# Optimization experiments

Measured on AMD Instinct MI355X. Metric: run time of the kernel, lower is better.

Reference implementation:

```python
import jax, jax.numpy as jnp
import numpy as np

N_NODES = 100000   # nodes per node type
N_EDGES = 800000   # edges per edge type
F_IN = 128         # lazy (-1,-1) input feature dim, chosen == hidden
HID = 128          # hidden_channels
OUT = 1            # out_channels
N_LAYERS = 2
B = 256            # batch_size (num graphs)
NEG_SLOPE = 0.2    # GATConv default leaky_relu slope


def setup_inputs() -> dict:
    key = jax.random.key(0)
    ks = jax.random.split(key, 16)
    x_i = jax.random.normal(ks[0], (N_NODES, F_IN), jnp.float32)
    x_j = jax.random.normal(ks[1], (N_NODES, F_IN), jnp.float32)
    ei_ii = jax.random.randint(ks[2], (2, N_EDGES), 0, N_NODES, jnp.int32)
    ei_jj = jax.random.randint(ks[3], (2, N_EDGES), 0, N_NODES, jnp.int32)
    ei_ij = jax.random.randint(ks[4], (2, N_EDGES), 0, N_NODES, jnp.int32)
    ei_ji = jax.random.randint(ks[5], (2, N_EDGES), 0, N_NODES, jnp.int32)
    batch_i = jnp.sort(jax.random.randint(ks[6], (N_NODES,), 0, B, jnp.int32))
    batch_j = jnp.sort(jax.random.randint(ks[7], (N_NODES,), 0, B, jnp.int32))
    s = 1.0 / np.sqrt(HID)
    Ws = jax.random.normal(ks[8], (N_LAYERS, 4, F_IN, HID), jnp.float32) * s
    Wd = jax.random.normal(ks[9], (N_LAYERS, 4, F_IN, HID), jnp.float32) * s
    att_s = jax.random.normal(ks[10], (N_LAYERS, 4, HID), jnp.float32) * s
    att_d = jax.random.normal(ks[11], (N_LAYERS, 4, HID), jnp.float32) * s
    bias = jnp.zeros((N_LAYERS, 4, HID), jnp.float32)
    lin_w = jax.random.normal(ks[12], (HID, OUT), jnp.float32) * s
    lin_b = jnp.zeros((OUT,), jnp.float32)
    return dict(x_i=x_i, x_j=x_j, ei_ii=ei_ii, ei_jj=ei_jj, ei_ij=ei_ij,
                ei_ji=ei_ji, batch_i=batch_i, batch_j=batch_j, Ws=Ws, Wd=Wd,
                att_s=att_s, att_d=att_d, bias=bias, lin_w=lin_w, lin_b=lin_b)


def gat_conv(x_src, x_dst, edge, W_s, W_d, a_s, a_d, b):
    """Single-head GATConv: gather -> edge attention -> segment softmax -> scatter."""
    src, dst = edge[0], edge[1]
    n_dst = x_dst.shape[0]
    hs = x_src @ W_s                      # [Ns, C]
    hd = x_dst @ W_d                      # [Nd, C]
    e = jax.nn.leaky_relu((hs * a_s).sum(-1)[src] + (hd * a_d).sum(-1)[dst],
                          NEG_SLOPE)      # [E]
    m = jax.ops.segment_max(e, dst, num_segments=n_dst)
    m = jnp.where(jnp.isfinite(m), m, 0.0)  # empty segments -> 0
    p = jnp.exp(e - m[dst])
    denom = jax.ops.segment_sum(p, dst, num_segments=n_dst)
    alpha = p / jnp.maximum(denom[dst], 1e-16)
    out = jax.ops.segment_sum(alpha[:, None] * hs[src], dst, num_segments=n_dst)
    return out + b


def mean_pool(x, batch, size):
    s = jax.ops.segment_sum(x, batch, num_segments=size)
    cnt = jax.ops.segment_sum(jnp.ones((x.shape[0],), x.dtype), batch,
                              num_segments=size)
    return s / jnp.maximum(cnt, 1.0)[:, None]


def reference(x_i, x_j, ei_ii, ei_jj, ei_ij, ei_ji, batch_i, batch_j,
              Ws, Wd, att_s, att_d, bias, lin_w, lin_b):
    xi, xj = x_i, x_j
    for l in range(N_LAYERS):
        # edge-type order: 0=inner_i, 1=inner_j, 2=outer_ij, 3=outer_ji
        out_i = (gat_conv(xi, xi, ei_ii, Ws[l, 0], Wd[l, 0], att_s[l, 0], att_d[l, 0], bias[l, 0])
                 + gat_conv(xj, xi, ei_ji, Ws[l, 3], Wd[l, 3], att_s[l, 3], att_d[l, 3], bias[l, 3]))
        out_j = (gat_conv(xj, xj, ei_jj, Ws[l, 1], Wd[l, 1], att_s[l, 1], att_d[l, 1], bias[l, 1])
                 + gat_conv(xi, xj, ei_ij, Ws[l, 2], Wd[l, 2], att_s[l, 2], att_d[l, 2], bias[l, 2]))
        xi, xj = jnp.tanh(out_i), jnp.tanh(out_j)
    p_i = mean_pool(xi, batch_i, B)       # [B, HID]
    p_j = mean_pool(xj, batch_j, B)       # [B, HID]
    x = 0.5 * (p_i + p_j)                 # mean over the stacked pair
    return jax.nn.sigmoid(x @ lin_w + lin_b)
```

## Files before the change

### kernel.cpp

```cpp
#include <hip/hip_runtime.h>


#define NEG_SLOPE 0.2f

typedef __attribute__((ext_vector_type(8))) short short8v;
typedef __attribute__((ext_vector_type(4))) float float4v;
typedef __attribute__((ext_vector_type(2))) float float2v;

__device__ __forceinline__ unsigned short f2bf(float f) {
  unsigned u = __float_as_uint(f);
  unsigned r = (u + 0x7FFFu + ((u >> 16) & 1u)) >> 16;
  return (unsigned short)r;
}
__device__ __forceinline__ unsigned pack2(float a, float b) {
  return (unsigned)f2bf(a) | ((unsigned)f2bf(b) << 16);
}
__device__ __forceinline__ float bflo(unsigned u) {
  return __uint_as_float(u << 16);
}
__device__ __forceinline__ float bfhi(unsigned u) {
  return __uint_as_float(u & 0xFFFF0000u);
}
__device__ __forceinline__ float rl_f(float x, int lane) {
  return __int_as_float(__builtin_amdgcn_readlane(__float_as_int(x), lane));
}
__device__ __forceinline__ int rl_i(int x, int lane) {
  return __builtin_amdgcn_readlane(x, lane);
}

__global__ __launch_bounds__(256) void w_to_bf16t(const float* __restrict__ W,
                                                  unsigned short* __restrict__ Wt) {
  __shared__ float buf[64][129];
  int b = blockIdx.x, t = threadIdx.x;
  const float* w = W + (size_t)b * 16384;
  unsigned short* o = Wt + (size_t)b * 16384;
  for (int h = 0; h < 2; ++h) {
    for (int i = 0; i < 32; ++i) {
      int idx = i * 256 + t;
      buf[idx >> 7][idx & 127] = w[(size_t)(h * 64 + (idx >> 7)) * 128 + (idx & 127)];
    }
    __syncthreads();
    for (int i = 0; i < 32; ++i) {
      int idx = i * 256 + t;
      o[(size_t)(idx >> 6) * 128 + h * 64 + (idx & 63)] = f2bf(buf[idx & 63][idx >> 6]);
    }
    __syncthreads();
  }
}

__global__ void precompute_wa(const float* __restrict__ W,
                              const float* __restrict__ att,
                              float* __restrict__ out) {
  int idx = blockIdx.x;
  int f = threadIdx.x;
  const float* w = W + (size_t)idx * 128 * 128 + (size_t)f * 128;
  const float* a = att + idx * 128;
  float s = 0.f;
  #pragma unroll 8
  for (int h = 0; h < 128; ++h) s += w[h] * a[h];
  out[idx * 128 + f] = s;
}

struct GemmArgs {
  const unsigned short* Wt1; const float* att1;
  unsigned char* Hb1; float* as1;
  const unsigned short* Wt2; const float* att2;
  unsigned char* Hb2; float* as2;
  const float* vdA; const float* vdB;
  float* adA; float* adB;
};

template <int XBF16>
__global__ __launch_bounds__(256) void gemm_dual2(
    const void* __restrict__ X0, const void* __restrict__ X1,
    GemmArgs Ga, GemmArgs Gb, int M) {
  __shared__ unsigned short Xt[64][136];
  __shared__ unsigned short Wt[128][136];
  const int t = threadIdx.x;
  const int row0 = blockIdx.x * 64;
  const void* Xv = blockIdx.y ? X1 : X0;
  const GemmArgs& G = blockIdx.y ? Gb : Ga;

  {
    int r = t >> 2;
    int cq = (t & 3) * 32;
    int gr = row0 + r;
    if (gr >= M) gr = M - 1;
    if (XBF16) {
      const unsigned short* Xb = (const unsigned short*)Xv;
      const uint4* src = (const uint4*)(Xb + (size_t)gr * 128 + cq);
      #pragma unroll
      for (int i = 0; i < 4; ++i) *(uint4*)&Xt[r][cq + i * 8] = src[i];
    } else {
      const float* Xf = (const float*)Xv;
      const float4* src = (const float4*)(Xf + (size_t)gr * 128 + cq);
      #pragma unroll
      for (int i = 0; i < 8; ++i) {
        float4 v = src[i];
        uint2 u;
        u.x = pack2(v.x, v.y);
        u.y = pack2(v.z, v.w);
        *(uint2*)&Xt[r][cq + i * 4] = u;
      }
    }
  }
  {
    int n = t >> 1;
    int kh = (t & 1) * 64;
    const uint4* src = (const uint4*)(G.Wt1 + (size_t)n * 128 + kh);
    #pragma unroll
    for (int i = 0; i < 8; ++i) *(uint4*)&Wt[n][kh + i * 8] = src[i];
  }
  __syncthreads();

  if (t < 128) {
    int r = t & 63;
    const float* vd = (t < 64) ? G.vdA : G.vdB;
    float* adout = (t < 64) ? G.adA : G.adB;
    float sum = 0.f;
    #pragma unroll 4
    for (int k8 = 0; k8 < 16; ++k8) {
      uint4 u = *(const uint4*)&Xt[r][k8 * 8];
      const float* v = vd + k8 * 8;
      sum = fmaf(bflo(u.x), v[0], sum);
      sum = fmaf(bfhi(u.x), v[1], sum);
      sum = fmaf(bflo(u.y), v[2], sum);
      sum = fmaf(bfhi(u.y), v[3], sum);
      sum = fmaf(bflo(u.z), v[4], sum);
      sum = fmaf(bfhi(u.z), v[5], sum);
      sum = fmaf(bflo(u.w), v[6], sum);
      sum = fmaf(bfhi(u.w), v[7], sum);
    }
    int gr = row0 + r;
    if (gr < M) adout[gr] = sum;
  }

  const int lane = t & 63;
  const int wv = t >> 6;
  const int m = lane & 15;
  const int g = lane >> 4;
  const int ws = wv * 16;

  for (int ww = 0; ww < 2; ++ww) {
    if (ww == 1) {
      __syncthreads();
      int n = t >> 1;
      int kh = (t & 1) * 64;
      const uint4* src = (const uint4*)(G.Wt2 + (size_t)n * 128 + kh);
      #pragma unroll
      for (int i = 0; i < 8; ++i) *(uint4*)&Wt[n][kh + i * 8] = src[i];
      __syncthreads();
    }
    const float* att = ww ? G.att2 : G.att1;
    unsigned char* Hb = ww ? G.Hb2 : G.Hb1;
    float* as_ = ww ? G.as2 : G.as1;

    float4v acc[8];
    float4v z = {0.f, 0.f, 0.f, 0.f};
    #pragma unroll
    for (int nt = 0; nt < 8; ++nt) acc[nt] = z;

    #pragma unroll
    for (int ks = 0; ks < 4; ++ks) {
      short8v a = *(const short8v*)&Xt[ws + m][ks * 32 + g * 8];
      #pragma unroll
      for (int nt = 0; nt < 8; ++nt) {
        short8v b = *(const short8v*)&Wt[nt * 16 + m][ks * 32 + g * 8];
        acc[nt] = __builtin_amdgcn_mfma_f32_16x16x32_bf16(a, b, acc[nt], 0, 0, 0);
      }
    }

    {
      float attv[8];
      #pragma unroll
      for (int nt = 0; nt < 8; ++nt) attv[nt] = att[nt * 16 + m];
      #pragma unroll
      for (int r = 0; r < 4; ++r) {
        float s = 0.f;
        #pragma unroll
        for (int nt = 0; nt < 8; ++nt) s = fmaf(acc[nt][r], attv[nt], s);
        #pragma unroll
        for (int off = 1; off < 16; off <<= 1) s += __shfl_xor(s, off);
        if (m == 0) {
          int grow = row0 + ws + g * 4 + r;
          if (grow < M) as_[grow] = s;
        }
      }
    }

    #pragma unroll
    for (int nt = 0; nt < 8; ++nt) {
      #pragma unroll
      for (int r = 0; r < 4; ++r) {
        float v = acc[nt][r];
        float vn = __shfl_xor(v, 1);
        if ((m & 1) == 0) {
          int grow = row0 + ws + g * 4 + r;
          if (grow < M) {
            int pk = __builtin_amdgcn_cvt_pk_fp8_f32(v, vn, 0, false);
            *(unsigned short*)(Hb + (size_t)grow * 128 + nt * 16 + m) =
                (unsigned short)(pk & 0xFFFF);
          }
        }
      }
    }
  }
}

__global__ void hist4(const int* __restrict__ e0, const int* __restrict__ e1,
                      const int* __restrict__ e2, const int* __restrict__ e3,
                      int E, int* __restrict__ deg, int N) {
  int t = blockIdx.y;
  const int* ei = (t == 0) ? e0 : (t == 1) ? e1 : (t == 2) ? e2 : e3;
  int stride = gridDim.x * 256;
  for (int i = blockIdx.x * 256 + threadIdx.x; i < E; i += stride)
    atomicAdd(&deg[t * N + ei[E + i]], 1);
}

__global__ __launch_bounds__(1024) void scan4(const int* __restrict__ deg,
                                              int* __restrict__ rowptr, int N) {
  __shared__ int sums[1024];
  int t = threadIdx.x;
  int ty = blockIdx.x;
  const int* d = deg + (size_t)ty * N;
  int* rp = rowptr + (size_t)ty * (N + 1);
  int chunk = (N + 1023) / 1024;
  int lo = t * chunk;
  int hi = lo + chunk; if (hi > N) hi = N; if (lo > N) lo = N;
  int s = 0;
  for (int i = lo; i < hi; ++i) s += d[i];
  sums[t] = s;
  __syncthreads();
  for (int off = 1; off < 1024; off <<= 1) {
    int add = (t >= off) ? sums[t - off] : 0;
    __syncthreads();
    sums[t] += add;
    __syncthreads();
  }
  int run = (t == 0) ? 0 : sums[t - 1];
  for (int i = lo; i < hi; ++i) {
    rp[i] = run;
    run += d[i];
  }
  if (t == 1023) rp[N] = sums[1023];
}

__global__ void fill4(const int* __restrict__ e0, const int* __restrict__ e1,
                      const int* __restrict__ e2, const int* __restrict__ e3,
                      int E, const int* __restrict__ rowptr,
                      int* __restrict__ fill, int* __restrict__ csrc, int N) {
  int t = blockIdx.y;
  const int* ei = (t == 0) ? e0 : (t == 1) ? e1 : (t == 2) ? e2 : e3;
  int stride = gridDim.x * 256;
  for (int i = blockIdx.x * 256 + threadIdx.x; i < E; i += stride) {
    int d = ei[E + i];
    int s = ei[i];
    int pos = rowptr[(size_t)t * (N + 1) + d] + atomicAdd(&fill[t * N + d], 1);
    csrc[(size_t)t * E + pos] = s;
  }
}

struct PairArgs {
  const int* rA; const int* sA; const unsigned char* hA;
  const float* asA; const float* adA;
  const int* rB; const int* sB; const unsigned char* hB;
  const float* asB; const float* adB;
  const float* biasA; const float* biasB;
};

#define GATH(P_h, idx, dst) {                                           \
  unsigned short uu = *(const unsigned short*)((P_h) + (size_t)(idx) * 128 + lane * 2); \
  dst = __builtin_amdgcn_cvt_pk_f32_fp8((int)uu, false); }

__device__ __forceinline__ void agg_pair(const PairArgs& P, int n, int lane,
                                         float2& outA, float2& outB) {
  int begA = P.rA[n], endA = P.rA[n + 1];
  int begB = P.rB[n], endB = P.rB[n + 1];
  float adA = P.adA[n], adB = P.adB[n];
  float lsA = 0.f, lsB = 0.f;
  float2 aA = make_float2(0.f, 0.f), aB = make_float2(0.f, 0.f);
  int cA = begA, cB = begB;
  while (cA < endA || cB < endB) {
    int kA = cA + lane, kB = cB + lane;
    bool vA = kA < endA;
    bool vB = kB < endB;
    int sA = vA ? P.sA[kA] : 0;
    int sB = vB ? P.sB[kB] : 0;
    float eA = vA ? (P.asA[sA] + adA) : 0.f;
    float eB = vB ? (P.asB[sB] + adB) : 0.f;
    eA = eA > 0.f ? eA : NEG_SLOPE * eA;
    eB = eB > 0.f ? eB : NEG_SLOPE * eB;
    float pA = vA ? __expf(eA) : 0.f;
    float pB = vB ? __expf(eB) : 0.f;
    int cntA = endA - cA; cntA = cntA < 0 ? 0 : (cntA > 64 ? 64 : cntA);
    int cntB = endB - cB; cntB = cntB < 0 ? 0 : (cntB > 64 ? 64 : cntB);
    int cnt = cntA > cntB ? cntA : cntB;
    for (int base = 0; base < cnt; base += 8) {
      float qa0 = rl_f(pA, base + 0), qa1 = rl_f(pA, base + 1);
      float qa2 = rl_f(pA, base + 2), qa3 = rl_f(pA, base + 3);
      float qa4 = rl_f(pA, base + 4), qa5 = rl_f(pA, base + 5);
      float qa6 = rl_f(pA, base + 6), qa7 = rl_f(pA, base + 7);
      float qb0 = rl_f(pB, base + 0), qb1 = rl_f(pB, base + 1);
      float qb2 = rl_f(pB, base + 2), qb3 = rl_f(pB, base + 3);
      float qb4 = rl_f(pB, base + 4), qb5 = rl_f(pB, base + 5);
      float qb6 = rl_f(pB, base + 6), qb7 = rl_f(pB, base + 7);
      int ta0 = rl_i(sA, base + 0), ta1 = rl_i(sA, base + 1);
      int ta2 = rl_i(sA, base + 2), ta3 = rl_i(sA, base + 3);
      int ta4 = rl_i(sA, base + 4), ta5 = rl_i(sA, base + 5);
      int ta6 = rl_i(sA, base + 6), ta7 = rl_i(sA, base + 7);
      int tb0 = rl_i(sB, base + 0), tb1 = rl_i(sB, base + 1);
      int tb2 = rl_i(sB, base + 2), tb3 = rl_i(sB, base + 3);
      int tb4 = rl_i(sB, base + 4), tb5 = rl_i(sB, base + 5);
      int tb6 = rl_i(sB, base + 6), tb7 = rl_i(sB, base + 7);
      float2v ha0, ha1, ha2, ha3, ha4, ha5, ha6, ha7;
      float2v hb0, hb1, hb2, hb3, hb4, hb5, hb6, hb7;
      GATH(P.hA, ta0, ha0) GATH(P.hA, ta1, ha1)
      GATH(P.hA, ta2, ha2) GATH(P.hA, ta3, ha3)
      GATH(P.hA, ta4, ha4) GATH(P.hA, ta5, ha5)
      GATH(P.hA, ta6, ha6) GATH(P.hA, ta7, ha7)
      GATH(P.hB, tb0, hb0) GATH(P.hB, tb1, hb1)
      GATH(P.hB, tb2, hb2) GATH(P.hB, tb3, hb3)
      GATH(P.hB, tb4, hb4) GATH(P.hB, tb5, hb5)
      GATH(P.hB, tb6, hb6) GATH(P.hB, tb7, hb7)
      lsA += ((qa0 + qa1) + (qa2 + qa3)) + ((qa4 + qa5) + (qa6 + qa7));
      lsB += ((qb0 + qb1) + (qb2 + qb3)) + ((qb4 + qb5) + (qb6 + qb7));
      aA.x = fmaf(qa0, ha0[0], aA.x); aA.y = fmaf(qa0, ha0[1], aA.y);
      aA.x = fmaf(qa1, ha1[0], aA.x); aA.y = fmaf(qa1, ha1[1], aA.y);
      aA.x = fmaf(qa2, ha2[0], aA.x); aA.y = fmaf(qa2, ha2[1], aA.y);
      aA.x = fmaf(qa3, ha3[0], aA.x); aA.y = fmaf(qa3, ha3[1], aA.y);
      aA.x = fmaf(qa4, ha4[0], aA.x); aA.y = fmaf(qa4, ha4[1], aA.y);
      aA.x = fmaf(qa5, ha5[0], aA.x); aA.y = fmaf(qa5, ha5[1], aA.y);
      aA.x = fmaf(qa6, ha6[0], aA.x); aA.y = fmaf(qa6, ha6[1], aA.y);
      aA.x = fmaf(qa7, ha7[0], aA.x); aA.y = fmaf(qa7, ha7[1], aA.y);
      aB.x = fmaf(qb0, hb0[0], aB.x); aB.y = fmaf(qb0, hb0[1], aB.y);
      aB.x = fmaf(qb1, hb1[0], aB.x); aB.y = fmaf(qb1, hb1[1], aB.y);
      aB.x = fmaf(qb2, hb2[0], aB.x); aB.y = fmaf(qb2, hb2[1], aB.y);
      aB.x = fmaf(qb3, hb3[0], aB.x); aB.y = fmaf(qb3, hb3[1], aB.y);
      aB.x = fmaf(qb4, hb4[0], aB.x); aB.y = fmaf(qb4, hb4[1], aB.y);
      aB.x = fmaf(qb5, hb5[0], aB.x); aB.y = fmaf(qb5, hb5[1], aB.y);
      aB.x = fmaf(qb6, hb6[0], aB.x); aB.y = fmaf(qb6, hb6[1], aB.y);
      aB.x = fmaf(qb7, hb7[0], aB.x); aB.y = fmaf(qb7, hb7[1], aB.y);
    }
    cA += 64;
    cB += 64;
  }
  float invA = 1.f / fmaxf(lsA, 1e-16f);
  float invB = 1.f / fmaxf(lsB, 1e-16f);
  outA = make_float2(aA.x * invA, aA.y * invA);
  outB = make_float2(aB.x * invB, aB.y * invB);
}

__global__ __launch_bounds__(256) void agg_store2(
    PairArgs P0, unsigned short* __restrict__ out0,
    PairArgs P1, unsigned short* __restrict__ out1, int N) {
  int wave = (blockIdx.x * 256 + threadIdx.x) >> 6;
  int lane = threadIdx.x & 63;
  if (wave >= N) return;
  const PairArgs& P = blockIdx.y ? P1 : P0;
  unsigned short* out = blockIdx.y ? out1 : out0;
  float2 a, b;
  agg_pair(P, wave, lane, a, b);
  float2 b1 = *(const float2*)(P.biasA + lane * 2);
  float2 b2 = *(const float2*)(P.biasB + lane * 2);
  float vx = tanhf(a.x + b.x + b1.x + b2.x);
  float vy = tanhf(a.y + b.y + b1.y + b2.y);
  *(unsigned*)(out + (size_t)wave * 128 + lane * 2) = pack2(vx, vy);
}

__global__ __launch_bounds__(256) void agg_pool2(
    PairArgs P0, const int* __restrict__ batch0, float* __restrict__ pool0,
    PairArgs P1, const int* __restrict__ batch1, float* __restrict__ pool1,
    int N) {
  int wave = (blockIdx.x * 256 + threadIdx.x) >> 6;
  int lane = threadIdx.x & 63;
  if (wave >= N) return;
  const PairArgs& P = blockIdx.y ? P1 : P0;
  const int* batch = blockIdx.y ? batch1 : batch0;
  float* pool = blockIdx.y ? pool1 : pool0;
  float2 a, b;
  agg_pair(P, wave, lane, a, b);
  float2 b1 = *(const float2*)(P.biasA + lane * 2);
  float2 b2 = *(const float2*)(P.biasB + lane * 2);
  float vx = tanhf(a.x + b.x + b1.x + b2.x);
  float vy = tanhf(a.y + b.y + b1.y + b2.y);
  int bb = batch[wave];
  float* p = pool + (size_t)bb * 128 + lane * 2;
  unsafeAtomicAdd(p, vx);
  unsafeAtomicAdd(p + 1, vy);
}

__device__ __forceinline__ int lower_bound_i(const int* __restrict__ a, int n,
                                             int v) {
  int lo = 0, hi = n;
  while (lo < hi) {
    int mid = (lo + hi) >> 1;
    if (a[mid] < v) lo = mid + 1; else hi = mid;
  }
  return lo;
}

__global__ void final_k(const float* __restrict__ pool_i,
                        const int* __restrict__ batch_i,
                        const float* __restrict__ pool_j,
                        const int* __restrict__ batch_j, int N,
                        const float* __restrict__ lin_w,
                        const float* __restrict__ lin_b,
                        float* __restrict__ out) {
  int b = threadIdx.x;
  float ci = (float)(lower_bound_i(batch_i, N, b + 1) -
                     lower_bound_i(batch_i, N, b));
  float cj = (float)(lower_bound_i(batch_j, N, b + 1) -
                     lower_bound_i(batch_j, N, b));
  ci = fmaxf(ci, 1.f);
  cj = fmaxf(cj, 1.f);
  float acc = 0.f;
  #pragma unroll 4
  for (int f = 0; f < 128; ++f) {
    float x = 0.5f * (pool_i[(size_t)b * 128 + f] / ci +
                      pool_j[(size_t)b * 128 + f] / cj);
    acc += x * lin_w[f];
  }
  acc += lin_b[0];
  out[b] = 1.f / (1.f + __expf(-acc));
}

extern "C" void kernel_launch(void* const* d_in, const int* in_sizes, int n_in,
                              void* d_out, int out_size, void* d_ws,
                              size_t ws_size, hipStream_t stream) {
  const float* x_i = (const float*)d_in[0];
  const float* x_j = (const float*)d_in[1];
  const int* ei_arr[4] = {(const int*)d_in[2], (const int*)d_in[3],
                          (const int*)d_in[4], (const int*)d_in[5]};
  const int* batch_i = (const int*)d_in[6];
  const int* batch_j = (const int*)d_in[7];
  const float* Ws = (const float*)d_in[8];
  const float* Wd = (const float*)d_in[9];
  const float* att_s = (const float*)d_in[10];
  const float* att_d = (const float*)d_in[11];
  const float* bias = (const float*)d_in[12];
  const float* lin_w = (const float*)d_in[13];
  const float* lin_b = (const float*)d_in[14];
  float* out = (float*)d_out;

  const int N = in_sizes[0] / 128;
  const int E = in_sizes[2] / 2;
  const size_t NF = (size_t)N * 128;

  char* w = (char*)d_ws;
  auto alloc = [&](size_t bytes) {
    char* p = w;
    w += (bytes + 255) & ~(size_t)255;
    return p;
  };
  unsigned short* bufA_i = (unsigned short*)alloc(NF * 2);
  unsigned short* bufA_j = (unsigned short*)alloc(NF * 2);
  unsigned char* hsb[4];
  for (int c = 0; c < 4; ++c) hsb[c] = (unsigned char*)alloc(NF);
  int* csrc = (int*)alloc((size_t)4 * E * 4);
  int* rowptr = (int*)alloc((size_t)4 * (N + 1) * 4);
  int* deg = (int*)alloc((size_t)4 * N * 4);
  int* fillc = (int*)alloc((size_t)4 * N * 4);
  float* asb[4];
  for (int c = 0; c < 4; ++c) asb[c] = (float*)alloc((size_t)N * 4);
  float* adb[4];
  for (int c = 0; c < 4; ++c) adb[c] = (float*)alloc((size_t)N * 4);
  float* wdad = (float*)alloc(8 * 128 * 4);
  unsigned short* Wst = (unsigned short*)alloc(8 * 16384 * 2);
  float* pool = (float*)alloc(2 * 256 * 128 * 4);
  float* pool_i = pool;
  float* pool_j = pool + 256 * 128;

  w_to_bf16t<<<8, 256, 0, stream>>>(Ws, Wst);
  precompute_wa<<<8, 128, 0, stream>>>(Wd, att_d, wdad);

  hipMemsetAsync(deg, 0, (size_t)4 * N * 4, stream);
  hipMemsetAsync(fillc, 0, (size_t)4 * N * 4, stream);
  dim3 egrid(512, 4);
  hist4<<<egrid, 256, 0, stream>>>(ei_arr[0], ei_arr[1], ei_arr[2], ei_arr[3],
                                   E, deg, N);
  scan4<<<4, 1024, 0, stream>>>(deg, rowptr, N);
  fill4<<<egrid, 256, 0, stream>>>(ei_arr[0], ei_arr[1], ei_arr[2], ei_arr[3],
                                   E, rowptr, fillc, csrc, N);

  hipMemsetAsync(pool, 0, 2 * 256 * 128 * 4, stream);

  const int gemm_blocks = (N + 63) / 64;
  const int nodew_blocks = (N + 3) / 4;

  for (int l = 0; l < 2; ++l) {
    const void* cur_i = (l == 0) ? (const void*)x_i : (const void*)bufA_i;
    const void* cur_j = (l == 0) ? (const void*)x_j : (const void*)bufA_j;
    const size_t L = (size_t)l * 4;

    GemmArgs Ga = {Wst + (L + 0) * 16384, att_s + (L + 0) * 128, hsb[0], asb[0],
                   Wst + (L + 2) * 16384, att_s + (L + 2) * 128, hsb[2], asb[2],
                   wdad + (L + 0) * 128, wdad + (L + 3) * 128, adb[0], adb[3]};
    GemmArgs Gb = {Wst + (L + 1) * 16384, att_s + (L + 1) * 128, hsb[1], asb[1],
                   Wst + (L + 3) * 16384, att_s + (L + 3) * 128, hsb[3], asb[3],
                   wdad + (L + 1) * 128, wdad + (L + 2) * 128, adb[1], adb[2]};
    dim3 ggrid(gemm_blocks, 2);
    if (l == 0) {
      gemm_dual2<0><<<ggrid, 256, 0, stream>>>(cur_i, cur_j, Ga, Gb, N);
    } else {
      gemm_dual2<1><<<ggrid, 256, 0, stream>>>(cur_i, cur_j, Ga, Gb, N);
    }

    PairArgs P0 = {rowptr + (size_t)0 * (N + 1), csrc + (size_t)0 * E, hsb[0],
                   asb[0], adb[0],
                   rowptr + (size_t)3 * (N + 1), csrc + (size_t)3 * E, hsb[3],
                   asb[3], adb[3],
                   bias + (L + 0) * 128, bias + (L + 3) * 128};
    PairArgs P1 = {rowptr + (size_t)1 * (N + 1), csrc + (size_t)1 * E, hsb[1],
                   asb[1], adb[1],
                   rowptr + (size_t)2 * (N + 1), csrc + (size_t)2 * E, hsb[2],
                   asb[2], adb[2],
                   bias + (L + 1) * 128, bias + (L + 2) * 128};

    dim3 agrid(nodew_blocks, 2);
    if (l == 0) {
      agg_store2<<<agrid, 256, 0, stream>>>(P0, bufA_i, P1, bufA_j, N);
    } else {
      agg_pool2<<<agrid, 256, 0, stream>>>(P0, batch_i, pool_i, P1, batch_j,
                                           pool_j, N);
    }
  }

  final_k<<<1, 256, 0, stream>>>(pool_i, batch_i, pool_j, batch_j, N, lin_w,
                                 lin_b, out);
}
```

Baseline: 1.036 ms.

## Split each wave into half-waves handling the two edge types in aggregation

```diff
diff --git a/kernel.cpp b/kernel.cpp
--- a/kernel.cpp
+++ b/kernel.cpp
@@ -20,9 +20,6 @@
 }
 __device__ __forceinline__ float bfhi(unsigned u) {
   return __uint_as_float(u & 0xFFFF0000u);
-}
-__device__ __forceinline__ float rl_f(float x, int lane) {
-  return __int_as_float(__builtin_amdgcn_readlane(__float_as_int(x), lane));
 }
 __device__ __forceinline__ int rl_i(int x, int lane) {
   return __builtin_amdgcn_readlane(x, lane);
@@ -268,86 +265,70 @@
   const float* biasA; const float* biasB;
 };
 
-#define GATH(P_h, idx, dst) {                                           \
-  unsigned short uu = *(const unsigned short*)((P_h) + (size_t)(idx) * 128 + lane * 2); \
-  dst = __builtin_amdgcn_cvt_pk_f32_fp8((int)uu, false); }
-
-__device__ __forceinline__ void agg_pair(const PairArgs& P, int n, int lane,
-                                         float2& outA, float2& outB) {
-  int begA = P.rA[n], endA = P.rA[n + 1];
-  int begB = P.rB[n], endB = P.rB[n + 1];
-  float adA = P.adA[n], adB = P.adB[n];
-  float lsA = 0.f, lsB = 0.f;
-  float2 aA = make_float2(0.f, 0.f), aB = make_float2(0.f, 0.f);
-  int cA = begA, cB = begB;
-  while (cA < endA || cB < endB) {
-    int kA = cA + lane, kB = cB + lane;
-    bool vA = kA < endA;
-    bool vB = kB < endB;
-    int sA = vA ? P.sA[kA] : 0;
-    int sB = vB ? P.sB[kB] : 0;
-    float eA = vA ? (P.asA[sA] + adA) : 0.f;
-    float eB = vB ? (P.asB[sB] + adB) : 0.f;
-    eA = eA > 0.f ? eA : NEG_SLOPE * eA;
-    eB = eB > 0.f ? eB : NEG_SLOPE * eB;
-    float pA = vA ? __expf(eA) : 0.f;
-    float pB = vB ? __expf(eB) : 0.f;
-    int cntA = endA - cA; cntA = cntA < 0 ? 0 : (cntA > 64 ? 64 : cntA);
-    int cntB = endB - cB; cntB = cntB < 0 ? 0 : (cntB > 64 ? 64 : cntB);
+__device__ __forceinline__ void agg_pair_hw(const PairArgs& P, int n, int lane,
+                                            float* accv) {
+  const int half = lane >> 5;
+  const int hl = lane & 31;
+  const int hbase = lane & 32;
+  const int* rp = half ? P.rB : P.rA;
+  const int* sc = half ? P.sB : P.sA;
+  const unsigned char* hp = half ? P.hB : P.hA;
+  const float* asp = half ? P.asB : P.asA;
+  const float ad = (half ? P.adB : P.adA)[n];
+  int beg = rp[n], end = rp[n + 1];
+  float lsum = 0.f;
+  float a0 = 0.f, a1 = 0.f, a2 = 0.f, a3 = 0.f;
+  int c = beg;
+  while (true) {
+    int cl = end - c;
+    cl = cl < 0 ? 0 : (cl > 32 ? 32 : cl);
+    int cntA = rl_i(cl, 0);
+    int cntB = rl_i(cl, 32);
     int cnt = cntA > cntB ? cntA : cntB;
+    if (cnt == 0) break;
+    int k = c + hl;
+    bool valid = k < end;
+    int s = valid ? sc[k] : 0;
+    float e = valid ? (asp[s] + ad) : 0.f;
+    e = e > 0.f ? e : NEG_SLOPE * e;
+    float p = valid ? __expf(e) : 0.f;
     for (int base = 0; base < cnt; base += 8) {
-      float qa0 = rl_f(pA, base + 0), qa1 = rl_f(pA, base + 1);
-      float qa2 = rl_f(pA, base + 2), qa3 = rl_f(pA, base + 3);
-      float qa4 = rl_f(pA, base + 4), qa5 = rl_f(pA, base + 5);
-      float qa6 = rl_f(pA, base + 6), qa7 = rl_f(pA, base + 7);
-      float qb0 = rl_f(pB, base + 0), qb1 = rl_f(pB, base + 1);
-      float qb2 = rl_f(pB, base + 2), qb3 = rl_f(pB, base + 3);
-      float qb4 = rl_f(pB, base + 4), qb5 = rl_f(pB, base + 5);
-      float qb6 = rl_f(pB, base + 6), qb7 = rl_f(pB, base + 7);
-      int ta0 = rl_i(sA, base + 0), ta1 = rl_i(sA, base + 1);
-      int ta2 = rl_i(sA, base + 2), ta3 = rl_i(sA, base + 3);
-      int ta4 = rl_i(sA, base + 4), ta5 = rl_i(sA, base + 5);
-      int ta6 = rl_i(sA, base + 6), ta7 = rl_i(sA, base + 7);
-      int tb0 = rl_i(sB, base + 0), tb1 = rl_i(sB, base + 1);
-      int tb2 = rl_i(sB, base + 2), tb3 = rl_i(sB, base + 3);
-      int tb4 = rl_i(sB, base + 4), tb5 = rl_i(sB, base + 5);
-      int tb6 = rl_i(sB, base + 6), tb7 = rl_i(sB, base + 7);
-      float2v ha0, ha1, ha2, ha3, ha4, ha5, ha6, ha7;
-      float2v hb0, hb1, hb2, hb3, hb4, hb5, hb6, hb7;
-      GATH(P.hA, ta0, ha0) GATH(P.hA, ta1, ha1)
-      GATH(P.hA, ta2, ha2) GATH(P.hA, ta3, ha3)
-      GATH(P.hA, ta4, ha4) GATH(P.hA, ta5, ha5)
-      GATH(P.hA, ta6, ha6) GATH(P.hA, ta7, ha7)
-      GATH(P.hB, tb0, hb0) GATH(P.hB, tb1, hb1)
-      GATH(P.hB, tb2, hb2) GATH(P.hB, tb3, hb3)
-      GATH(P.hB, tb4, hb4) GATH(P.hB, tb5, hb5)
-      GATH(P.hB, tb6, hb6) GATH(P.hB, tb7, hb7)
-      lsA += ((qa0 + qa1) + (qa2 + qa3)) + ((qa4 + qa5) + (qa6 + qa7));
-      lsB += ((qb0 + qb1) + (qb2 + qb3)) + ((qb4 + qb5) + (qb6 + qb7));
-      aA.x = fmaf(qa0, ha0[0], aA.x); aA.y = fmaf(qa0, ha0[1], aA.y);
-      aA.x = fmaf(qa1, ha1[0], aA.x); aA.y = fmaf(qa1, ha1[1], aA.y);
-      aA.x = fmaf(qa2, ha2[0], aA.x); aA.y = fmaf(qa2, ha2[1], aA.y);
-      aA.x = fmaf(qa3, ha3[0], aA.x); aA.y = fmaf(qa3, ha3[1], aA.y);
-      aA.x = fmaf(qa4, ha4[0], aA.x); aA.y = fmaf(qa4, ha4[1], aA.y);
-      aA.x = fmaf(qa5, ha5[0], aA.x); aA.y = fmaf(qa5, ha5[1], aA.y);
-      aA.x = fmaf(qa6, ha6[0], aA.x); aA.y = fmaf(qa6, ha6[1], aA.y);
-      aA.x = fmaf(qa7, ha7[0], aA.x); aA.y = fmaf(qa7, ha7[1], aA.y);
-      aB.x = fmaf(qb0, hb0[0], aB.x); aB.y = fmaf(qb0, hb0[1], aB.y);
-      aB.x = fmaf(qb1, hb1[0], aB.x); aB.y = fmaf(qb1, hb1[1], aB.y);
-      aB.x = fmaf(qb2, hb2[0], aB.x); aB.y = fmaf(qb2, hb2[1], aB.y);
-      aB.x = fmaf(qb3, hb3[0], aB.x); aB.y = fmaf(qb3, hb3[1], aB.y);
-      aB.x = fmaf(qb4, hb4[0], aB.x); aB.y = fmaf(qb4, hb4[1], aB.y);
-      aB.x = fmaf(qb5, hb5[0], aB.x); aB.y = fmaf(qb5, hb5[1], aB.y);
-      aB.x = fmaf(qb6, hb6[0], aB.x); aB.y = fmaf(qb6, hb6[1], aB.y);
-      aB.x = fmaf(qb7, hb7[0], aB.x); aB.y = fmaf(qb7, hb7[1], aB.y);
-    }
-    cA += 64;
-    cB += 64;
-  }
-  float invA = 1.f / fmaxf(lsA, 1e-16f);
-  float invB = 1.f / fmaxf(lsB, 1e-16f);
-  outA = make_float2(aA.x * invA, aA.y * invA);
-  outB = make_float2(aB.x * invB, aB.y * invB);
+      int i0 = hbase + base;
+      float q0 = __shfl(p, i0 + 0), q1 = __shfl(p, i0 + 1);
+      float q2 = __shfl(p, i0 + 2), q3 = __shfl(p, i0 + 3);
+      float q4 = __shfl(p, i0 + 4), q5 = __shfl(p, i0 + 5);
+      float q6 = __shfl(p, i0 + 6), q7 = __shfl(p, i0 + 7);
+      int t0 = __shfl(s, i0 + 0), t1 = __shfl(s, i0 + 1);
+      int t2 = __shfl(s, i0 + 2), t3 = __shfl(s, i0 + 3);
+      int t4 = __shfl(s, i0 + 4), t5 = __shfl(s, i0 + 5);
+      int t6 = __shfl(s, i0 + 6), t7 = __shfl(s, i0 + 7);
+      unsigned u0 = *(const unsigned*)(hp + (size_t)t0 * 128 + hl * 4);
+      unsigned u1 = *(const unsigned*)(hp + (size_t)t1 * 128 + hl * 4);
+      unsigned u2 = *(const unsigned*)(hp + (size_t)t2 * 128 + hl * 4);
+      unsigned u3 = *(const unsigned*)(hp + (size_t)t3 * 128 + hl * 4);
+      unsigned u4 = *(const unsigned*)(hp + (size_t)t4 * 128 + hl * 4);
+      unsigned u5 = *(const unsigned*)(hp + (size_t)t5 * 128 + hl * 4);
+      unsigned u6 = *(const unsigned*)(hp + (size_t)t6 * 128 + hl * 4);
+      unsigned u7 = *(const unsigned*)(hp + (size_t)t7 * 128 + hl * 4);
+      lsum += ((q0 + q1) + (q2 + q3)) + ((q4 + q5) + (q6 + q7));
+      #define ACC4(q, u) {                                              \
+        float2v lo = __builtin_amdgcn_cvt_pk_f32_fp8((int)(u), false);  \
+        float2v hi = __builtin_amdgcn_cvt_pk_f32_fp8((int)(u), true);   \
+        a0 = fmaf(q, lo[0], a0); a1 = fmaf(q, lo[1], a1);               \
+        a2 = fmaf(q, hi[0], a2); a3 = fmaf(q, hi[1], a3); }
+      ACC4(q0, u0) ACC4(q1, u1) ACC4(q2, u2) ACC4(q3, u3)
+      ACC4(q4, u4) ACC4(q5, u5) ACC4(q6, u6) ACC4(q7, u7)
+      #undef ACC4
+    }
+    c += 32;
+  }
+  float inv = 1.f / fmaxf(lsum, 1e-16f);
+  a0 *= inv; a1 *= inv; a2 *= inv; a3 *= inv;
+  a0 += __shfl_xor(a0, 32);
+  a1 += __shfl_xor(a1, 32);
+  a2 += __shfl_xor(a2, 32);
+  a3 += __shfl_xor(a3, 32);
+  accv[0] = a0; accv[1] = a1; accv[2] = a2; accv[3] = a3;
 }
 
 __global__ __launch_bounds__(256) void agg_store2(
@@ -358,13 +339,21 @@
   if (wave >= N) return;
   const PairArgs& P = blockIdx.y ? P1 : P0;
   unsigned short* out = blockIdx.y ? out1 : out0;
-  float2 a, b;
-  agg_pair(P, wave, lane, a, b);
-  float2 b1 = *(const float2*)(P.biasA + lane * 2);
-  float2 b2 = *(const float2*)(P.biasB + lane * 2);
-  float vx = tanhf(a.x + b.x + b1.x + b2.x);
-  float vy = tanhf(a.y + b.y + b1.y + b2.y);
-  *(unsigned*)(out + (size_t)wave * 128 + lane * 2) = pack2(vx, vy);
+  float v[4];
+  agg_pair_hw(P, wave, lane, v);
+  if (lane < 32) {
+    int hl = lane;
+    float4 ba = *(const float4*)(P.biasA + hl * 4);
+    float4 bb = *(const float4*)(P.biasB + hl * 4);
+    float v0 = tanhf(v[0] + ba.x + bb.x);
+    float v1 = tanhf(v[1] + ba.y + bb.y);
+    float v2 = tanhf(v[2] + ba.z + bb.z);
+    float v3 = tanhf(v[3] + ba.w + bb.w);
+    uint2 o;
+    o.x = pack2(v0, v1);
+    o.y = pack2(v2, v3);
+    *(uint2*)(out + (size_t)wave * 128 + hl * 4) = o;
+  }
 }
 
 __global__ __launch_bounds__(256) void agg_pool2(
@@ -377,16 +366,19 @@
   const PairArgs& P = blockIdx.y ? P1 : P0;
   const int* batch = blockIdx.y ? batch1 : batch0;
   float* pool = blockIdx.y ? pool1 : pool0;
-  float2 a, b;
-  agg_pair(P, wave, lane, a, b);
-  float2 b1 = *(const float2*)(P.biasA + lane * 2);
-  float2 b2 = *(const float2*)(P.biasB + lane * 2);
-  float vx = tanhf(a.x + b.x + b1.x + b2.x);
-  float vy = tanhf(a.y + b.y + b1.y + b2.y);
-  int bb = batch[wave];
-  float* p = pool + (size_t)bb * 128 + lane * 2;
-  unsafeAtomicAdd(p, vx);
-  unsafeAtomicAdd(p + 1, vy);
+  float v[4];
+  agg_pair_hw(P, wave, lane, v);
+  if (lane < 32) {
+    int hl = lane;
+    float4 ba = *(const float4*)(P.biasA + hl * 4);
+    float4 bb = *(const float4*)(P.biasB + hl * 4);
+    int bb_idx = batch[wave];
+    float* p = pool + (size_t)bb_idx * 128 + hl * 4;
+    unsafeAtomicAdd(p + 0, tanhf(v[0] + ba.x + bb.x));
+    unsafeAtomicAdd(p + 1, tanhf(v[1] + ba.y + bb.y));
+    unsafeAtomicAdd(p + 2, tanhf(v[2] + ba.z + bb.z));
+    unsafeAtomicAdd(p + 3, tanhf(v[3] + ba.w + bb.w));
+  }
 }
 
 __device__ __forceinline__ int lower_bound_i(const int* __restrict__ a, int n,
```

New measurement: 2.077 ms. +100.6%, slower.

## Precompute per-edge attention weights into packed CSR before aggregation

Applied to the files above, without the earlier changes.

```diff
diff --git a/kernel.cpp b/kernel.cpp
--- a/kernel.cpp
+++ b/kernel.cpp
@@ -248,23 +248,44 @@
 __global__ void fill4(const int* __restrict__ e0, const int* __restrict__ e1,
                       const int* __restrict__ e2, const int* __restrict__ e3,
                       int E, const int* __restrict__ rowptr,
-                      int* __restrict__ fill, int* __restrict__ csrc, int N) {
+                      int* __restrict__ fill, int* __restrict__ epos, int N) {
   int t = blockIdx.y;
   const int* ei = (t == 0) ? e0 : (t == 1) ? e1 : (t == 2) ? e2 : e3;
   int stride = gridDim.x * 256;
   for (int i = blockIdx.x * 256 + threadIdx.x; i < E; i += stride) {
     int d = ei[E + i];
+    int pos = rowptr[(size_t)t * (N + 1) + d] + atomicAdd(&fill[t * N + d], 1);
+    epos[(size_t)t * E + i] = pos;
+  }
+}
+
+__global__ void edge_p4(const int* __restrict__ e0, const int* __restrict__ e1,
+                        const int* __restrict__ e2, const int* __restrict__ e3,
+                        int E, const int* __restrict__ epos,
+                        const float* __restrict__ as0, const float* __restrict__ as1,
+                        const float* __restrict__ as2, const float* __restrict__ as3,
+                        const float* __restrict__ ad0, const float* __restrict__ ad1,
+                        const float* __restrict__ ad2, const float* __restrict__ ad3,
+                        uint2* __restrict__ spcsr) {
+  int t = blockIdx.y;
+  const int* ei = (t == 0) ? e0 : (t == 1) ? e1 : (t == 2) ? e2 : e3;
+  const float* as_ = (t == 0) ? as0 : (t == 1) ? as1 : (t == 2) ? as2 : as3;
+  const float* ad_ = (t == 0) ? ad0 : (t == 1) ? ad1 : (t == 2) ? ad2 : ad3;
+  int stride = gridDim.x * 256;
+  for (int i = blockIdx.x * 256 + threadIdx.x; i < E; i += stride) {
     int s = ei[i];
-    int pos = rowptr[(size_t)t * (N + 1) + d] + atomicAdd(&fill[t * N + d], 1);
-    csrc[(size_t)t * E + pos] = s;
+    int d = ei[E + i];
+    float e = as_[s] + ad_[d];
+    e = e > 0.f ? e : NEG_SLOPE * e;
+    float p = __expf(e);
+    int k = epos[(size_t)t * E + i];
+    spcsr[(size_t)t * E + k] = make_uint2((unsigned)s, __float_as_uint(p));
   }
 }
 
 struct PairArgs {
-  const int* rA; const int* sA; const unsigned char* hA;
-  const float* asA; const float* adA;
-  const int* rB; const int* sB; const unsigned char* hB;
-  const float* asB; const float* adB;
+  const int* rA; const uint2* spA; const unsigned char* hA;
+  const int* rB; const uint2* spB; const unsigned char* hB;
   const float* biasA; const float* biasB;
 };
 
@@ -276,22 +297,17 @@
                                          float2& outA, float2& outB) {
   int begA = P.rA[n], endA = P.rA[n + 1];
   int begB = P.rB[n], endB = P.rB[n + 1];
-  float adA = P.adA[n], adB = P.adB[n];
   float lsA = 0.f, lsB = 0.f;
   float2 aA = make_float2(0.f, 0.f), aB = make_float2(0.f, 0.f);
   int cA = begA, cB = begB;
   while (cA < endA || cB < endB) {
     int kA = cA + lane, kB = cB + lane;
-    bool vA = kA < endA;
-    bool vB = kB < endB;
-    int sA = vA ? P.sA[kA] : 0;
-    int sB = vB ? P.sB[kB] : 0;
-    float eA = vA ? (P.asA[sA] + adA) : 0.f;
-    float eB = vB ? (P.asB[sB] + adB) : 0.f;
-    eA = eA > 0.f ? eA : NEG_SLOPE * eA;
-    eB = eB > 0.f ? eB : NEG_SLOPE * eB;
-    float pA = vA ? __expf(eA) : 0.f;
-    float pB = vB ? __expf(eB) : 0.f;
+    uint2 vAu = (kA < endA) ? P.spA[kA] : make_uint2(0u, 0u);
+    uint2 vBu = (kB < endB) ? P.spB[kB] : make_uint2(0u, 0u);
+    int sA = (int)vAu.x;
+    int sB = (int)vBu.x;
+    float pA = __uint_as_float(vAu.y);
+    float pB = __uint_as_float(vBu.y);
     int cntA = endA - cA; cntA = cntA < 0 ? 0 : (cntA > 64 ? 64 : cntA);
     int cntB = endB - cB; cntB = cntB < 0 ? 0 : (cntB > 64 ? 64 : cntB);
     int cnt = cntA > cntB ? cntA : cntB;
@@ -456,10 +472,11 @@
   unsigned short* bufA_j = (unsigned short*)alloc(NF * 2);
   unsigned char* hsb[4];
   for (int c = 0; c < 4; ++c) hsb[c] = (unsigned char*)alloc(NF);
-  int* csrc = (int*)alloc((size_t)4 * E * 4);
   int* rowptr = (int*)alloc((size_t)4 * (N + 1) * 4);
   int* deg = (int*)alloc((size_t)4 * N * 4);
   int* fillc = (int*)alloc((size_t)4 * N * 4);
+  int* epos = (int*)alloc((size_t)4 * E * 4);
+  uint2* spcsr = (uint2*)alloc((size_t)4 * E * 8);
   float* asb[4];
   for (int c = 0; c < 4; ++c) asb[c] = (float*)alloc((size_t)N * 4);
   float* adb[4];
@@ -480,7 +497,7 @@
                                    E, deg, N);
   scan4<<<4, 1024, 0, stream>>>(deg, rowptr, N);
   fill4<<<egrid, 256, 0, stream>>>(ei_arr[0], ei_arr[1], ei_arr[2], ei_arr[3],
-                                   E, rowptr, fillc, csrc, N);
+                                   E, rowptr, fillc, epos, N);
 
   hipMemsetAsync(pool, 0, 2 * 256 * 128 * 4, stream);
 
@@ -505,15 +522,16 @@
       gemm_dual2<1><<<ggrid, 256, 0, stream>>>(cur_i, cur_j, Ga, Gb, N);
     }
 
-    PairArgs P0 = {rowptr + (size_t)0 * (N + 1), csrc + (size_t)0 * E, hsb[0],
-                   asb[0], adb[0],
-                   rowptr + (size_t)3 * (N + 1), csrc + (size_t)3 * E, hsb[3],
-                   asb[3], adb[3],
+    edge_p4<<<egrid, 256, 0, stream>>>(
+        ei_arr[0], ei_arr[1], ei_arr[2], ei_arr[3], E, epos,
+        asb[0], asb[1], asb[2], asb[3],
+        adb[0], adb[1], adb[2], adb[3], spcsr);
+
+    PairArgs P0 = {rowptr + (size_t)0 * (N + 1), spcsr + (size_t)0 * E, hsb[0],
+                   rowptr + (size_t)3 * (N + 1), spcsr + (size_t)3 * E, hsb[3],
                    bias + (L + 0) * 128, bias + (L + 3) * 128};
-    PairArgs P1 = {rowptr + (size_t)1 * (N + 1), csrc + (size_t)1 * E, hsb[1],
-                   asb[1], adb[1],
-                   rowptr + (size_t)2 * (N + 1), csrc + (size_t)2 * E, hsb[2],
-                   asb[2], adb[2],
+    PairArgs P1 = {rowptr + (size_t)1 * (N + 1), spcsr + (size_t)1 * E, hsb[1],
+                   rowptr + (size_t)2 * (N + 1), spcsr + (size_t)2 * E, hsb[2],
                    bias + (L + 1) * 128, bias + (L + 2) * 128};
 
     dim3 agrid(nodew_blocks, 2);
```

After: 1.105 ms. 1.07x slower.
